# Kernel tuning notes

Measured on AMD Instinct MI355X. Metric: run time of the kernel, lower is better.

Reference implementation:

```python
import jax, jax.numpy as jnp
import numpy as np

N_NODES = 50000
N_EDGES = 800000
IN_DIM, HID_DIM, OUT_DIM = 128, 128, 256


def _gcn_conv(x, W, b, src, dst, num_nodes):
    # PyG GCNConv: h = D^{-1/2} (A + I) D^{-1/2} X W + b (self-loops already in src/dst)
    h = x @ W  # (N, F_out)
    ones = jnp.ones(src.shape[0], dtype=h.dtype)
    deg = jax.ops.segment_sum(ones, dst, num_segments=num_nodes)
    dinv = jnp.where(deg > 0, jax.lax.rsqrt(deg), 0.0)
    norm = dinv[src] * dinv[dst]  # (E,)
    msg = h[src] * norm[:, None]  # (E, F_out) gather
    out = jax.ops.segment_sum(msg, dst, num_segments=num_nodes)  # scatter-add
    return out + b


def setup_inputs() -> dict:
    key = jax.random.key(0)
    ks = jax.random.split(key, 6)
    x = jax.random.normal(ks[0], (N_NODES, IN_DIM), dtype=jnp.float32)
    edge_index = jax.random.randint(ks[1], (2, N_EDGES), 0, N_NODES, dtype=jnp.int64)
    W1 = jax.random.normal(ks[2], (IN_DIM, HID_DIM), dtype=jnp.float32) / np.sqrt(IN_DIM)
    b1 = jnp.zeros((HID_DIM,), jnp.float32)
    W2 = jax.random.normal(ks[3], (HID_DIM, OUT_DIM), dtype=jnp.float32) / np.sqrt(HID_DIM)
    b2 = jnp.zeros((OUT_DIM,), jnp.float32)
    Wa = jax.random.normal(ks[4], (OUT_DIM, 1), dtype=jnp.float32) / np.sqrt(OUT_DIM)
    ba = jnp.zeros((1,), jnp.float32)
    return {"x": x, "edge_index": edge_index, "W1": W1, "b1": b1, "W2": W2, "b2": b2, "Wa": Wa, "ba": ba}


def reference(x, edge_index, W1, b1, W2, b2, Wa, ba):
    n = x.shape[0]
    loops = jnp.arange(n, dtype=edge_index.dtype)
    src = jnp.concatenate([edge_index[0], loops])
    dst = jnp.concatenate([edge_index[1], loops])
    h = jax.nn.relu(_gcn_conv(x, W1, b1, src, dst, n))
    # dropout is a no-op in eval mode
    node_embeddings = jax.nn.relu(_gcn_conv(h, W2, b2, src, dst, n))
    logits = node_embeddings @ Wa + ba  # (N, 1)
    attn = jax.nn.softmax(logits, axis=0)  # softmax over nodes
    graph_embedding = jnp.sum(node_embeddings * attn, axis=0, keepdims=True)  # (1, OUT_DIM)
    return (node_embeddings, graph_embedding)
```

## Files before the change

kernel.cpp:

```cpp
#include <hip/hip_runtime.h>
#include <hip/hip_fp16.h>
#include <math.h>

typedef __attribute__((ext_vector_type(8))) short bf16x8;
typedef __attribute__((ext_vector_type(4))) float f32x4;

static __device__ __forceinline__ unsigned short f2bf(float x) {
    unsigned u = __float_as_uint(x);
    unsigned r = (u + 0x7FFF + ((u >> 16) & 1)) >> 16;
    return (unsigned short)r;
}
static __device__ __forceinline__ float bf2f(unsigned short h) {
    return __uint_as_float(((unsigned)h) << 16);
}
static __device__ __forceinline__ void addh8(float a[8], uint4 v) {
    float2 f;
    f = __half22float2(*(const __half2*)&v.x); a[0] += f.x; a[1] += f.y;
    f = __half22float2(*(const __half2*)&v.y); a[2] += f.x; a[3] += f.y;
    f = __half22float2(*(const __half2*)&v.z); a[4] += f.x; a[5] += f.y;
    f = __half22float2(*(const __half2*)&v.w); a[6] += f.x; a[7] += f.y;
}
static __device__ __forceinline__ void gll16(const unsigned short* g, unsigned short* l) {
    __builtin_amdgcn_global_load_lds(
        (const __attribute__((address_space(1))) unsigned int*)(const void*)g,
        (__attribute__((address_space(3))) unsigned int*)(void*)l, 16, 0, 0);
}


__global__ __launch_bounds__(256) void count_deg_kernel(const int* __restrict__ dst, int E,
                                                        int* __restrict__ deg,
                                                        int* __restrict__ epos) {
    int e = blockIdx.x * 256 + threadIdx.x;
    if (e < E) epos[e] = atomicAdd(&deg[dst[e]], 1);
}

__global__ __launch_bounds__(256) void scan_partial_kernel(const int* __restrict__ deg, int n,
                                                           int* __restrict__ partials) {
    int idx = blockIdx.x * 1024 + threadIdx.x * 4;
    int4 v = make_int4(0, 0, 0, 0);
    if (idx + 3 < n) v = *(const int4*)(deg + idx);
    else {
        if (idx < n) v.x = deg[idx];
        if (idx + 1 < n) v.y = deg[idx + 1];
        if (idx + 2 < n) v.z = deg[idx + 2];
    }
    int s = v.x + v.y + v.z + v.w;
    for (int off = 1; off < 64; off <<= 1) s += __shfl_xor(s, off);
    __shared__ int sm[4];
    int wave = threadIdx.x >> 6;
    if ((threadIdx.x & 63) == 0) sm[wave] = s;
    __syncthreads();
    if (threadIdx.x == 0) partials[blockIdx.x] = sm[0] + sm[1] + sm[2] + sm[3];
}

__global__ __launch_bounds__(64) void scan_offsets_kernel(const int* __restrict__ partials, int nb,
                                                          int* __restrict__ poff,
                                                          int* __restrict__ rowptr, int n) {
    int t = threadIdx.x;
    int v = (t < nb) ? partials[t] : 0;
    int s = v;
    for (int off = 1; off < 64; off <<= 1) {
        int u = __shfl_up(s, off);
        if (t >= off) s += u;
    }
    poff[t] = s - v;
    if (t == 63) rowptr[n] = s;
}

__global__ __launch_bounds__(256) void scan_final_kernel(const int* __restrict__ deg, int n,
                                                         const int* __restrict__ poff,
                                                         int* __restrict__ rowptr) {
    int idx = blockIdx.x * 1024 + threadIdx.x * 4;
    int4 v = make_int4(0, 0, 0, 0);
    if (idx + 3 < n) v = *(const int4*)(deg + idx);
    else {
        if (idx < n) v.x = deg[idx];
        if (idx + 1 < n) v.y = deg[idx + 1];
        if (idx + 2 < n) v.z = deg[idx + 2];
    }
    int tsum = v.x + v.y + v.z + v.w;
    int lane = threadIdx.x & 63, wave = threadIdx.x >> 6;
    int s = tsum;
    for (int off = 1; off < 64; off <<= 1) {
        int u = __shfl_up(s, off);
        if (lane >= off) s += u;
    }
    __shared__ int wsum[4];
    if (lane == 63) wsum[wave] = s;
    __syncthreads();
    int base = poff[blockIdx.x];
    for (int w = 0; w < wave; ++w) base += wsum[w];
    int e0 = base + s - tsum;
    int4 o;
    o.x = e0; o.y = e0 + v.x; o.z = o.y + v.y; o.w = o.z + v.z;
    if (idx + 3 < n) *(int4*)(rowptr + idx) = o;
    else {
        if (idx < n) rowptr[idx] = o.x;
        if (idx + 1 < n) rowptr[idx + 1] = o.y;
        if (idx + 2 < n) rowptr[idx + 2] = o.z;
    }
}


__global__ __launch_bounds__(256) void prep_kernel(
    const int* __restrict__ src, const int* __restrict__ dst, const int* __restrict__ epos, int E,
    const int* __restrict__ rowptr, int* __restrict__ csrsrc, int scatterBlocks,
    const float* __restrict__ x, const int* __restrict__ deg, float* __restrict__ dinv,
    __half2* __restrict__ xs16, int n, int prescaleBlocks,
    const float* __restrict__ W1, const float* __restrict__ W2,
    unsigned short* __restrict__ w1h, unsigned short* __restrict__ w1l,
    unsigned short* __restrict__ w2h, unsigned short* __restrict__ w2l) {
    int b = blockIdx.x;
    if (b < scatterBlocks) {
        int e = b * 256 + threadIdx.x;
        if (e < E) csrsrc[rowptr[dst[e]] + epos[e]] = src[e];
    } else if (b < scatterBlocks + prescaleBlocks) {
        int node = (b - scatterBlocks) * 4 + (threadIdx.x >> 6);
        int lane = threadIdx.x & 63;
        if (node >= n) return;
        float di = rsqrtf((float)(deg[node] + 1));
        if (lane == 0) dinv[node] = di;
        float2 v = *(const float2*)(x + (size_t)node * 128 + (lane << 1));
        xs16[(size_t)node * 64 + lane] = __floats2half2_rn(di * v.x, di * v.y);
    } else {
        int i = (b - scatterBlocks - prescaleBlocks) * 256 + threadIdx.x;
        if (i < 128 * 128) {
            int nn = i >> 7, k = i & 127;
            float v = W1[k * 128 + nn];
            unsigned short h = f2bf(v);
            int kp = (k & 64) + ((((k >> 3) & 7) ^ (nn & 7)) << 3) + (k & 7);
            w1h[nn * 128 + kp] = h;
            w1l[nn * 128 + kp] = f2bf(v - bf2f(h));
        } else if (i < 128 * 128 + 256 * 128) {
            int j = i - 128 * 128;
            int nn = j >> 7, k = j & 127;
            float v = W2[k * 256 + nn];
            unsigned short h = f2bf(v);
            int kp = (k & 64) + ((((k >> 3) & 7) ^ (nn & 7)) << 3) + (k & 7);
            w2h[nn * 128 + kp] = h;
            w2l[nn * 128 + kp] = f2bf(v - bf2f(h));
        }
    }
}


__global__ __launch_bounds__(256) void aggregate_kernel(const unsigned short* __restrict__ X16,
                                                        const float* __restrict__ dinv,
                                                        const int* __restrict__ rowptr,
                                                        const int* __restrict__ deg,
                                                        const int* __restrict__ csrsrc,
                                                        unsigned short* __restrict__ outH,
                                                        unsigned short* __restrict__ outL, int n) {
    int node = blockIdx.x * 16 + (threadIdx.x >> 4);
    int sl = threadIdx.x & 15;
    if (node >= n) return;
    const uint4* Xv = (const uint4*)X16;
    float acc[8] = {0.f, 0.f, 0.f, 0.f, 0.f, 0.f, 0.f, 0.f};
    addh8(acc, Xv[(size_t)node * 16 + sl]);
    int e0 = rowptr[node];
    int e1 = e0 + deg[node];
    int e = e0;
    for (; e + 4 <= e1; e += 4) {
        int s0 = csrsrc[e], s1 = csrsrc[e + 1], s2 = csrsrc[e + 2], s3 = csrsrc[e + 3];
        uint4 v0 = Xv[(size_t)s0 * 16 + sl];
        uint4 v1 = Xv[(size_t)s1 * 16 + sl];
        uint4 v2 = Xv[(size_t)s2 * 16 + sl];
        uint4 v3 = Xv[(size_t)s3 * 16 + sl];
        addh8(acc, v0); addh8(acc, v1); addh8(acc, v2); addh8(acc, v3);
    }
    for (; e < e1; ++e) {
        uint4 v = Xv[(size_t)csrsrc[e] * 16 + sl];
        addh8(acc, v);
    }
    float di = dinv[node];
    unsigned short h[8], l[8];
#pragma unroll
    for (int j = 0; j < 8; ++j) {
        float f = di * acc[j];
        h[j] = f2bf(f);
        l[j] = f2bf(f - bf2f(h[j]));
    }
    uint4 hv, lv;
    hv.x = (unsigned)h[0] | ((unsigned)h[1] << 16);
    hv.y = (unsigned)h[2] | ((unsigned)h[3] << 16);
    hv.z = (unsigned)h[4] | ((unsigned)h[5] << 16);
    hv.w = (unsigned)h[6] | ((unsigned)h[7] << 16);
    lv.x = (unsigned)l[0] | ((unsigned)l[1] << 16);
    lv.y = (unsigned)l[2] | ((unsigned)l[3] << 16);
    lv.z = (unsigned)l[4] | ((unsigned)l[5] << 16);
    lv.w = (unsigned)l[6] | ((unsigned)l[7] << 16);
    int pos = ((sl & 8) | ((sl & 7) ^ (node & 7))) * 8;
    *(uint4*)(outH + (size_t)node * 128 + pos) = hv;
    *(uint4*)(outL + (size_t)node * 128 + pos) = lv;
}


template <int N, bool SCALE_DINV, bool DO_LOGITS, bool OUT_F16>
__global__ __launch_bounds__(256, 2) void gemm_mfma(const unsigned short* __restrict__ Ah,
                                                    const unsigned short* __restrict__ Al,
                                                    const unsigned short* __restrict__ Bth,
                                                    const unsigned short* __restrict__ Btl,
                                                    const float* __restrict__ bias,
                                                    void* __restrict__ Cout, int M,
                                                    const float* __restrict__ dinv,
                                                    const float* __restrict__ Wa,
                                                    float* __restrict__ logits) {
    __shared__ unsigned short AsH[128 * 64];
    __shared__ unsigned short AsL[128 * 64];
    __shared__ unsigned short BsH[128 * 64];
    __shared__ unsigned short BsL[128 * 64];

    const int t = threadIdx.x;
    const int lane = t & 63;
    const int wave = t >> 6;
    const int wrow = wave >> 1;
    const int wcol = wave & 1;
    const int lq = lane >> 4;
    const int lm = lane & 15;
    const int row0 = blockIdx.x * 128;
    const int col0 = blockIdx.y * 128;

    const int lr = lane >> 3;
    const int p8 = (lane & 7) * 8;

    f32x4 acc[4][4] = {};
    float lacc[4][4] = {};

    for (int kc = 0; kc < 2; ++kc) {
        __syncthreads();
#pragma unroll
        for (int j = 0; j < 4; ++j) {
            int seg = wave * 4 + j;
            int r = seg * 8 + lr;
            size_t goA = (size_t)(row0 + r) * 128 + kc * 64 + p8;
            size_t goB = (size_t)(col0 + r) * 128 + kc * 64 + p8;
            gll16(Ah + goA, AsH + seg * 512);
            gll16(Al + goA, AsL + seg * 512);
            gll16(Bth + goB, BsH + seg * 512);
            gll16(Btl + goB, BsL + seg * 512);
        }
        __syncthreads();

#pragma unroll
        for (int ks = 0; ks < 2; ++ks) {
            bf16x8 ah[4], al[4], bh[4], bl[4];
            int gbase = ks * 4 + lq;
#pragma unroll
            for (int rt = 0; rt < 4; ++rt) {
                int ra = wrow * 64 + rt * 16 + lm;
                int off = ra * 64 + (gbase ^ (ra & 7)) * 8;
                ah[rt] = *(const bf16x8*)(AsH + off);
                al[rt] = *(const bf16x8*)(AsL + off);
            }
#pragma unroll
            for (int ct = 0; ct < 4; ++ct) {
                int nb = wcol * 64 + ct * 16 + lm;
                int off = nb * 64 + (gbase ^ (nb & 7)) * 8;
                bh[ct] = *(const bf16x8*)(BsH + off);
                bl[ct] = *(const bf16x8*)(BsL + off);
            }
#pragma unroll
            for (int rt = 0; rt < 4; ++rt)
#pragma unroll
                for (int ct = 0; ct < 4; ++ct) {
                    acc[rt][ct] = __builtin_amdgcn_mfma_f32_16x16x32_bf16(ah[rt], bh[ct], acc[rt][ct], 0, 0, 0);
                    acc[rt][ct] = __builtin_amdgcn_mfma_f32_16x16x32_bf16(al[rt], bh[ct], acc[rt][ct], 0, 0, 0);
                    acc[rt][ct] = __builtin_amdgcn_mfma_f32_16x16x32_bf16(ah[rt], bl[ct], acc[rt][ct], 0, 0, 0);
                }
        }
    }

#pragma unroll
    for (int ct = 0; ct < 4; ++ct) {
        int col = col0 + wcol * 64 + ct * 16 + lm;
        float bc = bias[col];
        float wac = DO_LOGITS ? Wa[col] : 0.f;
#pragma unroll
        for (int rt = 0; rt < 4; ++rt) {
            int rowb = row0 + wrow * 64 + rt * 16 + lq * 4;
#pragma unroll
            for (int reg = 0; reg < 4; ++reg) {
                int gr = rowb + reg;
                if (gr < M) {
                    float o = fmaxf(acc[rt][ct][reg] + bc, 0.f);
                    if (SCALE_DINV) o *= dinv[gr];
                    if (OUT_F16) ((__half*)Cout)[(size_t)gr * N + col] = __float2half(o);
                    else ((float*)Cout)[(size_t)gr * N + col] = o;
                    if (DO_LOGITS) lacc[rt][reg] += o * wac;
                }
            }
        }
    }

    if (DO_LOGITS) {
#pragma unroll
        for (int rt = 0; rt < 4; ++rt)
#pragma unroll
            for (int reg = 0; reg < 4; ++reg) {
                float s = lacc[rt][reg];
                s += __shfl_xor(s, 1);
                s += __shfl_xor(s, 2);
                s += __shfl_xor(s, 4);
                s += __shfl_xor(s, 8);
                int gr = row0 + wrow * 64 + rt * 16 + lq * 4 + reg;
                if (lm == 0 && gr < M) atomicAdd(&logits[gr], s);
            }
    }
}


__global__ __launch_bounds__(256) void maxsum_kernel(const float* __restrict__ logits, int n,
                                                     float2* __restrict__ part) {
    float m = -INFINITY, s = 0.f;
    for (int i = blockIdx.x * 256 + threadIdx.x; i < n; i += gridDim.x * 256) {
        float v = logits[i];
        if (v > m) { s = s * expf(m - v) + 1.f; m = v; }
        else s += expf(v - m);
    }
    __shared__ float sm[256], ss[256];
    sm[threadIdx.x] = m; ss[threadIdx.x] = s;
    __syncthreads();
    for (int off = 128; off > 0; off >>= 1) {
        if (threadIdx.x < off) {
            float m1 = sm[threadIdx.x], s1 = ss[threadIdx.x];
            float m2 = sm[threadIdx.x + off], s2 = ss[threadIdx.x + off];
            float M = fmaxf(m1, m2);
            sm[threadIdx.x] = M;
            ss[threadIdx.x] = s1 * expf(m1 - M) + s2 * expf(m2 - M);
        }
        __syncthreads();
    }
    if (threadIdx.x == 0) part[blockIdx.x] = make_float2(sm[0], ss[0]);
}

static __device__ __forceinline__ float2 merge_part(const float2* __restrict__ part, int t,
                                                    float* red2) {
    if (t < 64) {
        float2 p = part[t];
        float m = p.x, s = p.y;
        for (int off = 32; off > 0; off >>= 1) {
            float m2 = __shfl_xor(m, off);
            float s2 = __shfl_xor(s, off);
            float M = fmaxf(m, m2);
            s = s * expf(m - M) + s2 * expf(m2 - M);
            m = M;
        }
        if (t == 0) { red2[0] = m; red2[1] = s; }
    }
    __syncthreads();
    return make_float2(red2[0], red2[1]);
}

__global__ __launch_bounds__(256) void weighted_sum_kernel(const float* __restrict__ emb,
                                                           const float* __restrict__ logits,
                                                           const float2* __restrict__ part,
                                                           float* __restrict__ gpart, int n) {
    __shared__ float red2[2];
    float g = merge_part(part, threadIdx.x, red2).x;
    int wave = threadIdx.x >> 6;
    int lane = threadIdx.x & 63;
    int stride = gridDim.x * 4;
    float4 acc = make_float4(0.f, 0.f, 0.f, 0.f);
#pragma unroll 2
    for (int r = blockIdx.x * 4 + wave; r < n; r += stride) {
        float w = expf(logits[r] - g);
        float4 v = *(const float4*)(emb + (size_t)r * 256 + (lane << 2));
        acc.x += w * v.x; acc.y += w * v.y; acc.z += w * v.z; acc.w += w * v.w;
    }
    __shared__ float4 sm[256];
    sm[threadIdx.x] = acc;
    __syncthreads();
    if (wave == 0) {
        float4 a = sm[lane], b = sm[64 + lane], c = sm[128 + lane], d = sm[192 + lane];
        float4 s;
        s.x = (a.x + b.x) + (c.x + d.x);
        s.y = (a.y + b.y) + (c.y + d.y);
        s.z = (a.z + b.z) + (c.z + d.z);
        s.w = (a.w + b.w) + (c.w + d.w);
        *(float4*)(gpart + (size_t)blockIdx.x * 256 + (lane << 2)) = s;
    }
}

__global__ __launch_bounds__(256) void reduce_gpart_kernel(const float* __restrict__ gpart,
                                                           const float2* __restrict__ part,
                                                           float* __restrict__ outTail, int nb) {
    __shared__ float red2[2];
    float gsum = merge_part(part, threadIdx.x, red2).y;
    int rows = nb / gridDim.x;
    int r0 = blockIdx.x * rows;
    float s = 0.f;
    for (int r = r0; r < r0 + rows; ++r) s += gpart[(size_t)r * 256 + threadIdx.x];
    atomicAdd(&outTail[threadIdx.x], s / gsum);
}


extern "C" void kernel_launch(void* const* d_in, const int* in_sizes, int n_in,
                              void* d_out, int out_size, void* d_ws, size_t ws_size,
                              hipStream_t stream) {
    const float* x  = (const float*)d_in[0];
    const int* ei   = (const int*)d_in[1];
    const float* W1 = (const float*)d_in[2];
    const float* b1 = (const float*)d_in[3];
    const float* W2 = (const float*)d_in[4];
    const float* b2 = (const float*)d_in[5];
    const float* Wa = (const float*)d_in[6];
    float* out = (float*)d_out;

    const int n = in_sizes[0] / 128;
    const int E = in_sizes[1] / 2;
    const int* srcA = ei;
    const int* dstA = ei + E;
    const int nb = (n + 1023) / 1024;
    const int WS_BLOCKS = 1024;

    unsigned short* xs16 = (unsigned short*)d_ws;
    unsigned short* aggH = xs16 + (size_t)n * 128;
    unsigned short* aggL = aggH + (size_t)n * 128;
    unsigned short* w1h  = aggL + (size_t)n * 128;
    unsigned short* w1l  = w1h + 128 * 128;
    unsigned short* w2h  = w1l + 128 * 128;
    unsigned short* w2l  = w2h + 256 * 128;
    float* dinv   = (float*)(w2l + 256 * 128);
    float* logits = dinv + n;
    int* deg      = (int*)(logits + n);
    int* rowptr   = deg + n;
    int* partials = rowptr + n + 1;
    int* poff     = partials + 64;
    float2* part  = (float2*)(poff + 64);
    float* gpart  = (float*)(part + 64);
    int* epos     = (int*)(gpart + WS_BLOCKS * 256);
    int* csrsrc   = epos + E;

    hipMemsetAsync(logits, 0, sizeof(float) * (size_t)(2 * n), stream);
    hipMemsetAsync(out + (size_t)n * 256, 0, sizeof(float) * 256, stream);

    count_deg_kernel<<<(E + 255) / 256, 256, 0, stream>>>(dstA, E, deg, epos);
    scan_partial_kernel<<<nb, 256, 0, stream>>>(deg, n, partials);
    scan_offsets_kernel<<<1, 64, 0, stream>>>(partials, nb, poff, rowptr, n);
    scan_final_kernel<<<nb, 256, 0, stream>>>(deg, n, poff, rowptr);

    int scatterBlocks = (E + 255) / 256;
    int prescaleBlocks = (n + 3) / 4;
    int wconvBlocks = (128 * 128 + 256 * 128 + 255) / 256;
    prep_kernel<<<scatterBlocks + prescaleBlocks + wconvBlocks, 256, 0, stream>>>(
        srcA, dstA, epos, E, rowptr, csrsrc, scatterBlocks,
        x, deg, dinv, (__half2*)xs16, n, prescaleBlocks,
        W1, W2, w1h, w1l, w2h, w2l);

    int aggBlocks = (n + 15) / 16;
    int gemmRows = (n + 127) / 128;

    aggregate_kernel<<<aggBlocks, 256, 0, stream>>>(xs16, dinv, rowptr, deg, csrsrc, aggH, aggL, n);
    gemm_mfma<128, true, false, true><<<dim3(gemmRows, 1), 256, 0, stream>>>(
        aggH, aggL, w1h, w1l, b1, xs16, n, dinv, nullptr, nullptr);
    aggregate_kernel<<<aggBlocks, 256, 0, stream>>>(xs16, dinv, rowptr, deg, csrsrc, aggH, aggL, n);
    gemm_mfma<256, false, true, false><<<dim3(gemmRows, 2), 256, 0, stream>>>(
        aggH, aggL, w2h, w2l, b2, out, n, nullptr, Wa, logits);

    maxsum_kernel<<<64, 256, 0, stream>>>(logits, n, part);
    weighted_sum_kernel<<<WS_BLOCKS, 256, 0, stream>>>(out, logits, part, gpart, n);
    reduce_gpart_kernel<<<32, 256, 0, stream>>>(gpart, part, out + (size_t)n * 256, WS_BLOCKS);
}
```

Baseline: 296.5 us.

## Replicate degree counters eightfold to reduce atomic contention in CSR build

Degree counting now spreads its atomics over eight replicas of the degree array, indexed by edge id modulo eight. The scan kernels sum the replicas, and a new repsum kernel computes per-replica offsets so the scatter can place each edge. Aggregation and prescale now take degrees from rowptr differences instead of the deg array. This is meant to cut same-address atomic serialization, at the cost of an extra kernel launch, eight times more degree memory to memset and read, and an indirection through repOff.

```diff
diff --git a/kernel.cpp b/kernel.cpp
--- a/kernel.cpp
+++ b/kernel.cpp
@@ -27,24 +27,29 @@
 }
 
 
-__global__ __launch_bounds__(256) void count_deg_kernel(const int* __restrict__ dst, int E,
-                                                        int* __restrict__ deg,
+__global__ __launch_bounds__(256) void count_deg_kernel(const int* __restrict__ dst, int E, int n,
+                                                        int* __restrict__ degR,
                                                         int* __restrict__ epos) {
     int e = blockIdx.x * 256 + threadIdx.x;
-    if (e < E) epos[e] = atomicAdd(&deg[dst[e]], 1);
-}
-
-__global__ __launch_bounds__(256) void scan_partial_kernel(const int* __restrict__ deg, int n,
+    if (e < E) epos[e] = atomicAdd(&degR[(e & 7) * n + dst[e]], 1);
+}
+
+__global__ __launch_bounds__(256) void scan_partial_kernel(const int* __restrict__ degR, int n,
                                                            int* __restrict__ partials) {
     int idx = blockIdx.x * 1024 + threadIdx.x * 4;
-    int4 v = make_int4(0, 0, 0, 0);
-    if (idx + 3 < n) v = *(const int4*)(deg + idx);
-    else {
-        if (idx < n) v.x = deg[idx];
-        if (idx + 1 < n) v.y = deg[idx + 1];
-        if (idx + 2 < n) v.z = deg[idx + 2];
-    }
-    int s = v.x + v.y + v.z + v.w;
+    int s = 0;
+#pragma unroll
+    for (int r = 0; r < 8; ++r) {
+        const int* d = degR + (size_t)r * n;
+        int4 v = make_int4(0, 0, 0, 0);
+        if (idx + 3 < n) v = *(const int4*)(d + idx);
+        else {
+            if (idx < n) v.x = d[idx];
+            if (idx + 1 < n) v.y = d[idx + 1];
+            if (idx + 2 < n) v.z = d[idx + 2];
+        }
+        s += v.x + v.y + v.z + v.w;
+    }
     for (int off = 1; off < 64; off <<= 1) s += __shfl_xor(s, off);
     __shared__ int sm[4];
     int wave = threadIdx.x >> 6;
@@ -67,18 +72,24 @@
     if (t == 63) rowptr[n] = s;
 }
 
-__global__ __launch_bounds__(256) void scan_final_kernel(const int* __restrict__ deg, int n,
+__global__ __launch_bounds__(256) void scan_final_kernel(const int* __restrict__ degR, int n,
                                                          const int* __restrict__ poff,
                                                          int* __restrict__ rowptr) {
     int idx = blockIdx.x * 1024 + threadIdx.x * 4;
-    int4 v = make_int4(0, 0, 0, 0);
-    if (idx + 3 < n) v = *(const int4*)(deg + idx);
-    else {
-        if (idx < n) v.x = deg[idx];
-        if (idx + 1 < n) v.y = deg[idx + 1];
-        if (idx + 2 < n) v.z = deg[idx + 2];
-    }
-    int tsum = v.x + v.y + v.z + v.w;
+    int4 tv = make_int4(0, 0, 0, 0);
+#pragma unroll
+    for (int r = 0; r < 8; ++r) {
+        const int* d = degR + (size_t)r * n;
+        int4 v = make_int4(0, 0, 0, 0);
+        if (idx + 3 < n) v = *(const int4*)(d + idx);
+        else {
+            if (idx < n) v.x = d[idx];
+            if (idx + 1 < n) v.y = d[idx + 1];
+            if (idx + 2 < n) v.z = d[idx + 2];
+        }
+        tv.x += v.x; tv.y += v.y; tv.z += v.z; tv.w += v.w;
+    }
+    int tsum = tv.x + tv.y + tv.z + tv.w;
     int lane = threadIdx.x & 63, wave = threadIdx.x >> 6;
     int s = tsum;
     for (int off = 1; off < 64; off <<= 1) {
@@ -92,7 +103,7 @@
     for (int w = 0; w < wave; ++w) base += wsum[w];
     int e0 = base + s - tsum;
     int4 o;
-    o.x = e0; o.y = e0 + v.x; o.z = o.y + v.y; o.w = o.z + v.z;
+    o.x = e0; o.y = e0 + tv.x; o.z = o.y + tv.y; o.w = o.z + tv.z;
     if (idx + 3 < n) *(int4*)(rowptr + idx) = o;
     else {
         if (idx < n) rowptr[idx] = o.x;
@@ -101,24 +112,37 @@
     }
 }
 
+__global__ __launch_bounds__(256) void repsum_kernel(const int* __restrict__ degR,
+                                                     const int* __restrict__ rowptr,
+                                                     int* __restrict__ repOff, int n) {
+    int d = blockIdx.x * 256 + threadIdx.x;
+    if (d >= n) return;
+    int base = rowptr[d];
+#pragma unroll
+    for (int r = 0; r < 8; ++r) {
+        repOff[(size_t)r * n + d] = base;
+        base += degR[(size_t)r * n + d];
+    }
+}
+
 
 __global__ __launch_bounds__(256) void prep_kernel(
     const int* __restrict__ src, const int* __restrict__ dst, const int* __restrict__ epos, int E,
-    const int* __restrict__ rowptr, int* __restrict__ csrsrc, int scatterBlocks,
-    const float* __restrict__ x, const int* __restrict__ deg, float* __restrict__ dinv,
-    __half2* __restrict__ xs16, int n, int prescaleBlocks,
+    int n, const int* __restrict__ repOff, int* __restrict__ csrsrc, int scatterBlocks,
+    const float* __restrict__ x, const int* __restrict__ rowptr, float* __restrict__ dinv,
+    __half2* __restrict__ xs16, int prescaleBlocks,
     const float* __restrict__ W1, const float* __restrict__ W2,
     unsigned short* __restrict__ w1h, unsigned short* __restrict__ w1l,
     unsigned short* __restrict__ w2h, unsigned short* __restrict__ w2l) {
     int b = blockIdx.x;
     if (b < scatterBlocks) {
         int e = b * 256 + threadIdx.x;
-        if (e < E) csrsrc[rowptr[dst[e]] + epos[e]] = src[e];
+        if (e < E) csrsrc[repOff[(size_t)(e & 7) * n + dst[e]] + epos[e]] = src[e];
     } else if (b < scatterBlocks + prescaleBlocks) {
         int node = (b - scatterBlocks) * 4 + (threadIdx.x >> 6);
         int lane = threadIdx.x & 63;
         if (node >= n) return;
-        float di = rsqrtf((float)(deg[node] + 1));
+        float di = rsqrtf((float)(rowptr[node + 1] - rowptr[node] + 1));
         if (lane == 0) dinv[node] = di;
         float2 v = *(const float2*)(x + (size_t)node * 128 + (lane << 1));
         xs16[(size_t)node * 64 + lane] = __floats2half2_rn(di * v.x, di * v.y);
@@ -147,7 +171,6 @@
 __global__ __launch_bounds__(256) void aggregate_kernel(const unsigned short* __restrict__ X16,
                                                         const float* __restrict__ dinv,
                                                         const int* __restrict__ rowptr,
-                                                        const int* __restrict__ deg,
                                                         const int* __restrict__ csrsrc,
                                                         unsigned short* __restrict__ outH,
                                                         unsigned short* __restrict__ outL, int n) {
@@ -158,7 +181,7 @@
     float acc[8] = {0.f, 0.f, 0.f, 0.f, 0.f, 0.f, 0.f, 0.f};
     addh8(acc, Xv[(size_t)node * 16 + sl]);
     int e0 = rowptr[node];
-    int e1 = e0 + deg[node];
+    int e1 = rowptr[node + 1];
     int e = e0;
     for (; e + 4 <= e1; e += 4) {
         int s0 = csrsrc[e], s1 = csrsrc[e + 1], s2 = csrsrc[e + 2], s3 = csrsrc[e + 3];
@@ -422,38 +445,40 @@
     unsigned short* w2l  = w2h + 256 * 128;
     float* dinv   = (float*)(w2l + 256 * 128);
     float* logits = dinv + n;
-    int* deg      = (int*)(logits + n);
-    int* rowptr   = deg + n;
-    int* partials = rowptr + n + 1;
+    int* degR     = (int*)(logits + n);
+    int* rowptr   = degR + (size_t)8 * n;
+    int* repOff   = rowptr + n + 1;
+    int* partials = repOff + (size_t)8 * n;
     int* poff     = partials + 64;
     float2* part  = (float2*)(poff + 64);
     float* gpart  = (float*)(part + 64);
     int* epos     = (int*)(gpart + WS_BLOCKS * 256);
     int* csrsrc   = epos + E;
 
-    hipMemsetAsync(logits, 0, sizeof(float) * (size_t)(2 * n), stream);
+    hipMemsetAsync(logits, 0, sizeof(float) * (size_t)(9 * n), stream);
     hipMemsetAsync(out + (size_t)n * 256, 0, sizeof(float) * 256, stream);
 
-    count_deg_kernel<<<(E + 255) / 256, 256, 0, stream>>>(dstA, E, deg, epos);
-    scan_partial_kernel<<<nb, 256, 0, stream>>>(deg, n, partials);
+    count_deg_kernel<<<(E + 255) / 256, 256, 0, stream>>>(dstA, E, n, degR, epos);
+    scan_partial_kernel<<<nb, 256, 0, stream>>>(degR, n, partials);
     scan_offsets_kernel<<<1, 64, 0, stream>>>(partials, nb, poff, rowptr, n);
-    scan_final_kernel<<<nb, 256, 0, stream>>>(deg, n, poff, rowptr);
+    scan_final_kernel<<<nb, 256, 0, stream>>>(degR, n, poff, rowptr);
+    repsum_kernel<<<(n + 255) / 256, 256, 0, stream>>>(degR, rowptr, repOff, n);
 
     int scatterBlocks = (E + 255) / 256;
     int prescaleBlocks = (n + 3) / 4;
     int wconvBlocks = (128 * 128 + 256 * 128 + 255) / 256;
     prep_kernel<<<scatterBlocks + prescaleBlocks + wconvBlocks, 256, 0, stream>>>(
-        srcA, dstA, epos, E, rowptr, csrsrc, scatterBlocks,
-        x, deg, dinv, (__half2*)xs16, n, prescaleBlocks,
+        srcA, dstA, epos, E, n, repOff, csrsrc, scatterBlocks,
+        x, rowptr, dinv, (__half2*)xs16, prescaleBlocks,
         W1, W2, w1h, w1l, w2h, w2l);
 
     int aggBlocks = (n + 15) / 16;
     int gemmRows = (n + 127) / 128;
 
-    aggregate_kernel<<<aggBlocks, 256, 0, stream>>>(xs16, dinv, rowptr, deg, csrsrc, aggH, aggL, n);
+    aggregate_kernel<<<aggBlocks, 256, 0, stream>>>(xs16, dinv, rowptr, csrsrc, aggH, aggL, n);
     gemm_mfma<128, true, false, true><<<dim3(gemmRows, 1), 256, 0, stream>>>(
         aggH, aggL, w1h, w1l, b1, xs16, n, dinv, nullptr, nullptr);
-    aggregate_kernel<<<aggBlocks, 256, 0, stream>>>(xs16, dinv, rowptr, deg, csrsrc, aggH, aggL, n);
+    aggregate_kernel<<<aggBlocks, 256, 0, stream>>>(xs16, dinv, rowptr, csrsrc, aggH, aggL, n);
     gemm_mfma<256, false, true, false><<<dim3(gemmRows, 2), 256, 0, stream>>>(
         aggH, aggL, w2h, w2l, b2, out, n, nullptr, Wa, logits);
 
```

Result: no change. 297.3 us (+0.3%).
